# Optimization experiments

Hardware: AMD Instinct MI355X
Metric: run time of the kernel (lower is better)

## Reference

```python
import jax, jax.numpy as jnp
import numpy as np

# pywt db2 decomposition filters (mode='symmetric', pywt defaults)
DEC_LO = np.array([-0.12940952255092145, 0.22414386804185735,
                   0.836516303737469, 0.48296291314469025], dtype=np.float32)
DEC_HI = np.array([-0.48296291314469025, 0.836516303737469,
                   -0.22414386804185735, -0.12940952255092145], dtype=np.float32)


def _dwt_axis(x, filt, axis):
    """Single-level 1D DWT along `axis`, symmetric padding, matching pywt.

    Equivalent to: symmetric-pad by F-1 each side, full convolution with
    `filt` (true convolution => filter flipped), take indices 1,3,5,...
    Implemented as pad (F-2, F-1) + strided correlation with reversed filter.
    """
    F = filt.shape[0]
    x = jnp.moveaxis(x, axis, -1)
    N = x.shape[-1]
    out_len = (N + F - 1) // 2
    pad = [(0, 0)] * (x.ndim - 1) + [(F - 2, F - 1)]
    xp = jnp.pad(x, pad, mode='symmetric')
    filt_rev = filt[::-1]
    # sum of 4 strided slices (F=4) -- fully vectorized, no big intermediates
    out = filt_rev[0] * xp[..., 0:2 * out_len:2]
    for k in range(1, F):
        out = out + filt_rev[k] * xp[..., k:k + 2 * out_len:2]
    return jnp.moveaxis(out, -1, axis)


def setup_inputs() -> dict:
    key = jax.random.key(0)
    x = jax.random.normal(key, (16, 3, 1024, 1024), dtype=jnp.float32)
    return {"x": x}


def reference(x):
    lo = jnp.asarray(DEC_LO)
    hi = jnp.asarray(DEC_HI)
    # pywt.dwt2 -> cA = 'aa' (approx rows, approx cols),
    #              cH = 'da' (detail along axis -2, approx along axis -1)
    lo_rows = _dwt_axis(x, lo, -2)
    hi_rows = _dwt_axis(x, hi, -2)
    cA = _dwt_axis(lo_rows, lo, -1)
    cH = _dwt_axis(hi_rows, lo, -1)
    return (cA, cH)
```

## Files before the change

kernel.cpp:

```cpp
#include <hip/hip_runtime.h>


#define N 1024
#define NOUT 513
#define TI 32
#define TJ 32
#define NROWS (2*TI + 2)
#define NCOLS 68
#define NQUAD (NCOLS/4)
#define EO 33

__device__ __forceinline__ int refl(int p) {
    int r = p - 2;
    r = (r < 0) ? (-1 - r) : r;
    r = (r > N - 1) ? (2 * N - 1 - r) : r;
    return r;
}

__global__ __launch_bounds__(256) void dwt2_fused(const float* __restrict__ x,
                                                  float* __restrict__ out) {
    const float lo_rev0 =  0.48296291314469025f;
    const float lo_rev1 =  0.836516303737469f;
    const float lo_rev2 =  0.22414386804185735f;
    const float lo_rev3 = -0.12940952255092145f;
    const float hi_rev0 = -0.12940952255092145f;
    const float hi_rev1 = -0.22414386804185735f;
    const float hi_rev2 =  0.836516303737469f;
    const float hi_rev3 = -0.48296291314469025f;

    __shared__ float xin[NROWS * NCOLS];
    __shared__ float lo_e[TI * EO];
    __shared__ float lo_o[TI * EO];
    __shared__ float hi_e[TI * EO];
    __shared__ float hi_o[TI * EO];

    const int tj_blk = blockIdx.x;
    const int ti_blk = blockIdx.y;
    const int img    = blockIdx.z;
    const int i0 = ti_blk * TI;
    const int j0 = tj_blk * TJ;
    const int t  = threadIdx.x;

    const float* xim = x + (size_t)img * N * N;

    int cb = 2 * j0 - 4;
    if (cb < 0) cb = 0;

    for (int v = t; v < NROWS * NQUAD; v += 256) {
        int rr = v / NQUAD;
        int q  = v - rr * NQUAD;
        int pr = 2 * i0 + rr;
        if (pr > N + 4) pr = N + 4;
        int row = refl(pr);
        int c0 = cb + 4 * q;
        float4 val;
        if (c0 + 3 < N) {
            val = *reinterpret_cast<const float4*>(xim + (size_t)row * N + c0);
        } else {
            float tmp0, tmp1, tmp2, tmp3;
            int c;
            c = c0 + 0; if (c > N - 1) c = N - 1; tmp0 = xim[(size_t)row * N + c];
            c = c0 + 1; if (c > N - 1) c = N - 1; tmp1 = xim[(size_t)row * N + c];
            c = c0 + 2; if (c > N - 1) c = N - 1; tmp2 = xim[(size_t)row * N + c];
            c = c0 + 3; if (c > N - 1) c = N - 1; tmp3 = xim[(size_t)row * N + c];
            val = make_float4(tmp0, tmp1, tmp2, tmp3);
        }
        *reinterpret_cast<float4*>(&xin[rr * NCOLS + 4 * q]) = val;
    }
    __syncthreads();

    for (int w = t; w < TI * 66; w += 256) {
        int ti = w / 66;
        int cc = w - ti * 66;
        int pc = 2 * j0 + cc;
        if (pc > N + 4) pc = N + 4;
        int lc = refl(pc) - cb;
        float a0 = xin[(2 * ti + 0) * NCOLS + lc];
        float a1 = xin[(2 * ti + 1) * NCOLS + lc];
        float a2 = xin[(2 * ti + 2) * NCOLS + lc];
        float a3 = xin[(2 * ti + 3) * NCOLS + lc];
        float lo = lo_rev0 * a0 + lo_rev1 * a1 + lo_rev2 * a2 + lo_rev3 * a3;
        float hi = hi_rev0 * a0 + hi_rev1 * a1 + hi_rev2 * a2 + hi_rev3 * a3;
        int e = cc >> 1;
        if (cc & 1) { lo_o[ti * EO + e] = lo; hi_o[ti * EO + e] = hi; }
        else        { lo_e[ti * EO + e] = lo; hi_e[ti * EO + e] = hi; }
    }
    __syncthreads();

    const size_t plane = (size_t)NOUT * NOUT;
    float* cA = out + (size_t)img * plane;
    float* cH = out + (size_t)48 * plane + (size_t)img * plane;
    for (int w = t; w < TI * TJ; w += 256) {
        int ti = w >> 5;
        int tj = w & 31;
        int i = i0 + ti;
        int j = j0 + tj;
        if (i < NOUT && j < NOUT) {
            float e0 = lo_e[ti * EO + tj];
            float o0 = lo_o[ti * EO + tj];
            float e1 = lo_e[ti * EO + tj + 1];
            float o1 = lo_o[ti * EO + tj + 1];
            float vA = lo_rev0 * e0 + lo_rev1 * o0 + lo_rev2 * e1 + lo_rev3 * o1;
            float f0 = hi_e[ti * EO + tj];
            float g0 = hi_o[ti * EO + tj];
            float f1 = hi_e[ti * EO + tj + 1];
            float g1 = hi_o[ti * EO + tj + 1];
            float vH = lo_rev0 * f0 + lo_rev1 * g0 + lo_rev2 * f1 + lo_rev3 * g1;
            cA[(size_t)i * NOUT + j] = vA;
            cH[(size_t)i * NOUT + j] = vH;
        }
    }
}

extern "C" void kernel_launch(void* const* d_in, const int* in_sizes, int n_in,
                              void* d_out, int out_size, void* d_ws, size_t ws_size,
                              hipStream_t stream) {
    (void)in_sizes; (void)n_in; (void)d_ws; (void)ws_size; (void)out_size;
    const float* x = (const float*)d_in[0];
    float* out = (float*)d_out;
    dim3 grid((NOUT + TJ - 1) / TJ, (NOUT + TI - 1) / TI, 48);
    dim3 block(256);
    dwt2_fused<<<grid, block, 0, stream>>>(x, out);
}
```

Measured before the change: 335.0 us.

## Replace 2D tiles with full-width row strips and register row streaming

Replaces the 32x32 2D tile kernel with a strip kernel where each block covers 8 output rows across the full 1024-column width. Each thread holds four input rows in registers and slides them down, reusing two rows per step instead of reloading halo rows. Vertical filter results go to double-buffered shared rows for the horizontal pass. This removes the column-halo redundancy and the reflection-heavy shared staging, but adds one barrier per output row and keeps a halo overlap of 2 rows per strip.

```diff
diff --git a/kernel.cpp b/kernel.cpp
--- a/kernel.cpp
+++ b/kernel.cpp
@@ -3,12 +3,8 @@
 
 #define N 1024
 #define NOUT 513
-#define TI 32
-#define TJ 32
-#define NROWS (2*TI + 2)
-#define NCOLS 68
-#define NQUAD (NCOLS/4)
-#define EO 33
+#define TI 8
+#define STRIPS ((NOUT + TI - 1) / TI)
 
 __device__ __forceinline__ int refl(int p) {
     int r = p - 2;
@@ -17,97 +13,80 @@
     return r;
 }
 
-__global__ __launch_bounds__(256) void dwt2_fused(const float* __restrict__ x,
-                                                  float* __restrict__ out) {
-    const float lo_rev0 =  0.48296291314469025f;
-    const float lo_rev1 =  0.836516303737469f;
-    const float lo_rev2 =  0.22414386804185735f;
-    const float lo_rev3 = -0.12940952255092145f;
-    const float hi_rev0 = -0.12940952255092145f;
-    const float hi_rev1 = -0.22414386804185735f;
-    const float hi_rev2 =  0.836516303737469f;
-    const float hi_rev3 = -0.48296291314469025f;
+__global__ __launch_bounds__(256, 8) void dwt2_strip(const float* __restrict__ x,
+                                                     float* __restrict__ out) {
+    const float l0 =  0.48296291314469025f;
+    const float l1 =  0.836516303737469f;
+    const float l2 =  0.22414386804185735f;
+    const float l3 = -0.12940952255092145f;
+    const float h0 = -0.12940952255092145f;
+    const float h1 = -0.22414386804185735f;
+    const float h2 =  0.836516303737469f;
+    const float h3 = -0.48296291314469025f;
 
-    __shared__ float xin[NROWS * NCOLS];
-    __shared__ float lo_e[TI * EO];
-    __shared__ float lo_o[TI * EO];
-    __shared__ float hi_e[TI * EO];
-    __shared__ float hi_o[TI * EO];
+    __shared__ float sLo[2][N];
+    __shared__ float sHi[2][N];
 
-    const int tj_blk = blockIdx.x;
-    const int ti_blk = blockIdx.y;
-    const int img    = blockIdx.z;
-    const int i0 = ti_blk * TI;
-    const int j0 = tj_blk * TJ;
+    const int strip = blockIdx.x;
+    const int img   = blockIdx.y;
+    const int i0 = strip * TI;
     const int t  = threadIdx.x;
+    const int c  = 4 * t;
 
     const float* xim = x + (size_t)img * N * N;
-
-    int cb = 2 * j0 - 4;
-    if (cb < 0) cb = 0;
-
-    for (int v = t; v < NROWS * NQUAD; v += 256) {
-        int rr = v / NQUAD;
-        int q  = v - rr * NQUAD;
-        int pr = 2 * i0 + rr;
-        if (pr > N + 4) pr = N + 4;
-        int row = refl(pr);
-        int c0 = cb + 4 * q;
-        float4 val;
-        if (c0 + 3 < N) {
-            val = *reinterpret_cast<const float4*>(xim + (size_t)row * N + c0);
-        } else {
-            float tmp0, tmp1, tmp2, tmp3;
-            int c;
-            c = c0 + 0; if (c > N - 1) c = N - 1; tmp0 = xim[(size_t)row * N + c];
-            c = c0 + 1; if (c > N - 1) c = N - 1; tmp1 = xim[(size_t)row * N + c];
-            c = c0 + 2; if (c > N - 1) c = N - 1; tmp2 = xim[(size_t)row * N + c];
-            c = c0 + 3; if (c > N - 1) c = N - 1; tmp3 = xim[(size_t)row * N + c];
-            val = make_float4(tmp0, tmp1, tmp2, tmp3);
-        }
-        *reinterpret_cast<float4*>(&xin[rr * NCOLS + 4 * q]) = val;
-    }
-    __syncthreads();
-
-    for (int w = t; w < TI * 66; w += 256) {
-        int ti = w / 66;
-        int cc = w - ti * 66;
-        int pc = 2 * j0 + cc;
-        if (pc > N + 4) pc = N + 4;
-        int lc = refl(pc) - cb;
-        float a0 = xin[(2 * ti + 0) * NCOLS + lc];
-        float a1 = xin[(2 * ti + 1) * NCOLS + lc];
-        float a2 = xin[(2 * ti + 2) * NCOLS + lc];
-        float a3 = xin[(2 * ti + 3) * NCOLS + lc];
-        float lo = lo_rev0 * a0 + lo_rev1 * a1 + lo_rev2 * a2 + lo_rev3 * a3;
-        float hi = hi_rev0 * a0 + hi_rev1 * a1 + hi_rev2 * a2 + hi_rev3 * a3;
-        int e = cc >> 1;
-        if (cc & 1) { lo_o[ti * EO + e] = lo; hi_o[ti * EO + e] = hi; }
-        else        { lo_e[ti * EO + e] = lo; hi_e[ti * EO + e] = hi; }
-    }
-    __syncthreads();
-
     const size_t plane = (size_t)NOUT * NOUT;
     float* cA = out + (size_t)img * plane;
-    float* cH = out + (size_t)48 * plane + (size_t)img * plane;
-    for (int w = t; w < TI * TJ; w += 256) {
-        int ti = w >> 5;
-        int tj = w & 31;
-        int i = i0 + ti;
-        int j = j0 + tj;
-        if (i < NOUT && j < NOUT) {
-            float e0 = lo_e[ti * EO + tj];
-            float o0 = lo_o[ti * EO + tj];
-            float e1 = lo_e[ti * EO + tj + 1];
-            float o1 = lo_o[ti * EO + tj + 1];
-            float vA = lo_rev0 * e0 + lo_rev1 * o0 + lo_rev2 * e1 + lo_rev3 * o1;
-            float f0 = hi_e[ti * EO + tj];
-            float g0 = hi_o[ti * EO + tj];
-            float f1 = hi_e[ti * EO + tj + 1];
-            float g1 = hi_o[ti * EO + tj + 1];
-            float vH = lo_rev0 * f0 + lo_rev1 * g0 + lo_rev2 * f1 + lo_rev3 * g1;
-            cA[(size_t)i * NOUT + j] = vA;
-            cH[(size_t)i * NOUT + j] = vH;
+    float* cH = out + ((size_t)48 + img) * plane;
+
+    const int nrows = (NOUT - i0 < TI) ? (NOUT - i0) : TI;
+
+    float4 r0 = *reinterpret_cast<const float4*>(xim + (size_t)refl(2 * i0)     * N + c);
+    float4 r1 = *reinterpret_cast<const float4*>(xim + (size_t)refl(2 * i0 + 1) * N + c);
+    float4 n0 = *reinterpret_cast<const float4*>(xim + (size_t)refl(2 * i0 + 2) * N + c);
+    float4 n1 = *reinterpret_cast<const float4*>(xim + (size_t)refl(2 * i0 + 3) * N + c);
+
+    for (int ii = 0; ii < nrows; ++ii) {
+        const int i = i0 + ii;
+        const int buf = ii & 1;
+
+        float4 lo, hi;
+        lo.x = l0 * r0.x + l1 * r1.x + l2 * n0.x + l3 * n1.x;
+        lo.y = l0 * r0.y + l1 * r1.y + l2 * n0.y + l3 * n1.y;
+        lo.z = l0 * r0.z + l1 * r1.z + l2 * n0.z + l3 * n1.z;
+        lo.w = l0 * r0.w + l1 * r1.w + l2 * n0.w + l3 * n1.w;
+        hi.x = h0 * r0.x + h1 * r1.x + h2 * n0.x + h3 * n1.x;
+        hi.y = h0 * r0.y + h1 * r1.y + h2 * n0.y + h3 * n1.y;
+        hi.z = h0 * r0.z + h1 * r1.z + h2 * n0.z + h3 * n1.z;
+        hi.w = h0 * r0.w + h1 * r1.w + h2 * n0.w + h3 * n1.w;
+        *reinterpret_cast<float4*>(&sLo[buf][c]) = lo;
+        *reinterpret_cast<float4*>(&sHi[buf][c]) = hi;
+        r0 = n0;
+        r1 = n1;
+
+        __syncthreads();
+
+        if (ii + 1 < nrows) {
+            const int ip = i + 1;
+            n0 = *reinterpret_cast<const float4*>(xim + (size_t)refl(2 * ip + 2) * N + c);
+            n1 = *reinterpret_cast<const float4*>(xim + (size_t)refl(2 * ip + 3) * N + c);
+        }
+
+        const float* __restrict__ Lrow = sLo[buf];
+        const float* __restrict__ Hrow = sHi[buf];
+        for (int j = t; j < NOUT; j += 256) {
+            float a0, a1, a2, a3, b0, b1, b2, b3;
+            if (j >= 1 && j <= NOUT - 2) {
+                const int cc = 2 * j - 2;
+                a0 = Lrow[cc]; a1 = Lrow[cc + 1]; a2 = Lrow[cc + 2]; a3 = Lrow[cc + 3];
+                b0 = Hrow[cc]; b1 = Hrow[cc + 1]; b2 = Hrow[cc + 2]; b3 = Hrow[cc + 3];
+            } else {
+                const int c0 = refl(2 * j), c1 = refl(2 * j + 1);
+                const int c2 = refl(2 * j + 2), c3 = refl(2 * j + 3);
+                a0 = Lrow[c0]; a1 = Lrow[c1]; a2 = Lrow[c2]; a3 = Lrow[c3];
+                b0 = Hrow[c0]; b1 = Hrow[c1]; b2 = Hrow[c2]; b3 = Hrow[c3];
+            }
+            cA[(size_t)i * NOUT + j] = l0 * a0 + l1 * a1 + l2 * a2 + l3 * a3;
+            cH[(size_t)i * NOUT + j] = l0 * b0 + l1 * b1 + l2 * b2 + l3 * b3;
         }
     }
 }
@@ -118,7 +97,7 @@
     (void)in_sizes; (void)n_in; (void)d_ws; (void)ws_size; (void)out_size;
     const float* x = (const float*)d_in[0];
     float* out = (float*)d_out;
-    dim3 grid((NOUT + TJ - 1) / TJ, (NOUT + TI - 1) / TI, 48);
+    dim3 grid(STRIPS, 48);
     dim3 block(256);
-    dwt2_fused<<<grid, block, 0, stream>>>(x, out);
+    dwt2_strip<<<grid, block, 0, stream>>>(x, out);
 }
```

New measurement: 312.7 us. -6.7%, faster.
